# Kernel optimization log

Hardware: AMD Instinct MI355X
Metric: run time of the kernel (lower is better)

## Reference

```python
import jax, jax.numpy as jnp
import numpy as np

B, C, IMG = 32, 3, 224
NP = 14            # patches per side
PS = IMG // NP     # 16
IN_DIM = C * PS * PS  # 768
D = 768
NH = 12
DH = D // NH       # 64
L = 12
MLP = 4 * D        # 3072
OUT = 1000
S = NP * NP + 1    # 197
EPS = 1e-5


def _pos_embedding(seq_len, dim):
    i = jnp.arange(seq_len, dtype=jnp.float32)[:, None]
    j = jnp.arange(dim, dtype=jnp.float32)[None, :]
    je = j - jnp.mod(j, 2.0)  # even: j, odd: j-1
    angle = i / jnp.power(10000.0, je / dim)
    return jnp.where(jnp.mod(j, 2.0) == 0, jnp.sin(angle), jnp.cos(angle))


def setup_inputs() -> dict:
    key = jax.random.key(0)
    ks = jax.random.split(key, 24)
    s = 0.02
    inp = {
        "x": jax.random.normal(ks[0], (B, C, IMG, IMG), jnp.float32),
        "cls_emb": jax.random.normal(ks[1], (1, 1, D), jnp.float32),
        "pos": _pos_embedding(S, D),
        "Wmap": jax.random.normal(ks[2], (IN_DIM, D), jnp.float32) * s,
        "bmap": jnp.zeros((D,), jnp.float32),
        "ln1_g": jnp.ones((L, D), jnp.float32),
        "ln1_b": jnp.zeros((L, D), jnp.float32),
        "Wq": jax.random.normal(ks[3], (L, NH, DH, DH), jnp.float32) * s,
        "bq": jnp.zeros((L, NH, DH), jnp.float32),
        "Wk": jax.random.normal(ks[4], (L, NH, DH, DH), jnp.float32) * s,
        "bk": jnp.zeros((L, NH, DH), jnp.float32),
        "Wv": jax.random.normal(ks[5], (L, NH, DH, DH), jnp.float32) * s,
        "bv": jnp.zeros((L, NH, DH), jnp.float32),
        "ln2_g": jnp.ones((L, D), jnp.float32),
        "ln2_b": jnp.zeros((L, D), jnp.float32),
        "W1": jax.random.normal(ks[6], (L, D, MLP), jnp.float32) * s,
        "b1": jnp.zeros((L, MLP), jnp.float32),
        "W2": jax.random.normal(ks[7], (L, MLP, D), jnp.float32) * s,
        "b2": jnp.zeros((L, D), jnp.float32),
        "Wc": jax.random.normal(ks[8], (D, OUT), jnp.float32) * s,
        "bc": jnp.zeros((OUT,), jnp.float32),
    }
    return inp


def _layernorm(x, g, b):
    mu = jnp.mean(x, axis=-1, keepdims=True)
    var = jnp.var(x, axis=-1, keepdims=True)
    return (x - mu) * jax.lax.rsqrt(var + EPS) * g + b


def _patchify(x):
    # [B,C,H,W] -> [B, NP*NP, C*PS*PS], flatten order (c, h, w) per patch
    n = x.shape[0]
    x = x.reshape(n, C, NP, PS, NP, PS)
    x = jnp.transpose(x, (0, 2, 4, 1, 3, 5))  # [B, ph, pw, C, PS, PS]
    return x.reshape(n, NP * NP, IN_DIM)


def reference(x, cls_emb, pos, Wmap, bmap, ln1_g, ln1_b, Wq, bq, Wk, bk, Wv, bv,
              ln2_g, ln2_b, W1, b1, W2, b2, Wc, bc):
    patches = _patchify(x)
    tokens = patches @ Wmap + bmap  # [B, NP*NP, D]
    tokens = jnp.concatenate([jnp.broadcast_to(cls_emb, (x.shape[0], 1, D)), tokens], axis=1)
    out = tokens + pos  # [B, S, D]
    scale = 1.0 / jnp.sqrt(jnp.float32(DH))
    for l in range(L):
        xn = _layernorm(out, ln1_g[l], ln1_b[l])
        xh = xn.reshape(xn.shape[0], S, NH, DH)
        q = jnp.einsum('bshd,hed->bshe', xh, Wq[l]) + bq[l]
        k = jnp.einsum('bshd,hed->bshe', xh, Wk[l]) + bk[l]
        v = jnp.einsum('bshd,hed->bshe', xh, Wv[l]) + bv[l]
        att = jax.nn.softmax(jnp.einsum('bqhd,bkhd->bhqk', q, k) * scale, axis=-1)
        attn_out = jnp.einsum('bhqk,bkhd->bqhd', att, v).reshape(out.shape)
        out = out + attn_out
        xn2 = _layernorm(out, ln2_g[l], ln2_b[l])
        h = jax.nn.gelu(xn2 @ W1[l] + b1[l], approximate=False)
        out = out + (h @ W2[l] + b2[l])
    cls = out[:, 0]
    return jax.nn.softmax(cls @ Wc + bc, axis=-1)
```

## Files before the change

kernel.cpp:

```cpp
#include <hip/hip_runtime.h>
#include <hip/hip_bf16.h>
#include <math.h>

#define VB   32
#define VD   768
#define VNH  12
#define VDH  64
#define VL   12
#define VMLP 3072
#define VOUT 1000
#define VS   197
#define VNPAT 196

typedef _Float16 half8 __attribute__((ext_vector_type(8)));
typedef _Float16 half4 __attribute__((ext_vector_type(4)));
typedef float f32x4 __attribute__((ext_vector_type(4)));

static __device__ __forceinline__ unsigned short f2h(float f) {
  _Float16 h = (_Float16)f;
  return __builtin_bit_cast(unsigned short, h);
}
static __device__ __forceinline__ float h2f(unsigned short u) {
  return (float)__builtin_bit_cast(_Float16, u);
}

__global__ __launch_bounds__(256) void patchify_kernel(
    const float* __restrict__ x, unsigned short* __restrict__ P) {
  int bp = blockIdx.x;
  int b = bp / VNPAT, p = bp - b * VNPAT;
  int py = p / 14, px = p - py * 14;
  int t = threadIdx.x;
  int iy = t >> 4, ix = t & 15;
#pragma unroll
  for (int c = 0; c < 3; c++) {
    float val = x[(((size_t)(b * 3 + c) * 224) + (py * 16 + iy)) * 224 + px * 16 + ix];
    P[(size_t)bp * 768 + c * 256 + t] = f2h(val);
  }
}

__global__ __launch_bounds__(256) void transpose_kernel(
    const float* __restrict__ W, unsigned short* __restrict__ WT,
    int K, int N) {
  __shared__ float ts[64][65];
  int n0 = blockIdx.x * 64, k0 = blockIdx.y * 64;
  const float* Wl = W + (size_t)blockIdx.z * K * N;
  unsigned short* WTl = WT + (size_t)blockIdx.z * K * N;
  int t = threadIdx.x;
  int r = t >> 4, c4 = (t & 15) * 4;
#pragma unroll
  for (int p = 0; p < 4; ++p) {
    int row = p * 16 + r;
    float4 v = *(const float4*)(Wl + (size_t)(k0 + row) * N + n0 + c4);
    ts[row][c4 + 0] = v.x; ts[row][c4 + 1] = v.y;
    ts[row][c4 + 2] = v.z; ts[row][c4 + 3] = v.w;
  }
  __syncthreads();
#pragma unroll
  for (int p = 0; p < 4; ++p) {
    int n = p * 16 + r;
    ushort4 o;
    o.x = f2h(ts[c4 + 0][n]);
    o.y = f2h(ts[c4 + 1][n]);
    o.z = f2h(ts[c4 + 2][n]);
    o.w = f2h(ts[c4 + 3][n]);
    *(ushort4*)(WTl + (size_t)(n0 + n) * K + k0 + c4) = o;
  }
}

__global__ __launch_bounds__(256) void pack_qkv_kernel(
    const float* __restrict__ Wq, const float* __restrict__ Wk,
    const float* __restrict__ Wv, unsigned short* __restrict__ Wp) {
  size_t idx = (size_t)blockIdx.x * 256 + threadIdx.x;
  int d = idx & 63;
  size_t r = idx >> 6;
  int n = (int)(r % 192);
  size_t lh = r / 192;
  int which = n >> 6, e = n & 63;
  const float* W = which == 0 ? Wq : which == 1 ? Wk : Wv;
  Wp[idx] = f2h(W[(lh * 64 + e) * 64 + d]);
}

__global__ __launch_bounds__(256) void addpos_kernel(
    const float* __restrict__ cls, const float* __restrict__ pos,
    float* __restrict__ out) {
  int bs = blockIdx.x;
  int s = bs % VS;
  int t = threadIdx.x;
  size_t o = (size_t)bs * VD;
#pragma unroll
  for (int j = 0; j < 3; j++) {
    int d = j * 256 + t;
    if (s == 0) out[o + d] = cls[d] + pos[d];
    else        out[o + d] += pos[(size_t)s * VD + d];
  }
}

__global__ __launch_bounds__(256) void ln_kernel(
    const float* __restrict__ x, unsigned short* __restrict__ y,
    const float* __restrict__ g, const float* __restrict__ b) {
  int row = blockIdx.x;
  int t = threadIdx.x;
  const float* xr = x + (size_t)row * VD;
  float v0 = xr[t], v1 = xr[t + 256], v2 = xr[t + 512];
  float s = v0 + v1 + v2;
  float ss = v0 * v0 + v1 * v1 + v2 * v2;
#pragma unroll
  for (int off = 32; off; off >>= 1) {
    s  += __shfl_down(s, off);
    ss += __shfl_down(ss, off);
  }
  __shared__ float red[10];
  int wid = t >> 6, lane = t & 63;
  if (lane == 0) { red[wid] = s; red[4 + wid] = ss; }
  __syncthreads();
  if (t == 0) {
    float S  = red[0] + red[1] + red[2] + red[3];
    float SS = red[4] + red[5] + red[6] + red[7];
    float mu = S * (1.0f / VD);
    float var = SS * (1.0f / VD) - mu * mu;
    red[8] = mu;
    red[9] = rsqrtf(var + 1e-5f);
  }
  __syncthreads();
  float mu = red[8], rs = red[9];
  unsigned short* yr = y + (size_t)row * VD;
  yr[t]       = f2h((v0 - mu) * rs * g[t]       + b[t]);
  yr[t + 256] = f2h((v1 - mu) * rs * g[t + 256] + b[t + 256]);
  yr[t + 512] = f2h((v2 - mu) * rs * g[t + 512] + b[t + 512]);
}

__global__ __launch_bounds__(256) void qkv_gemm(
    const unsigned short* __restrict__ xn,
    const unsigned short* __restrict__ Wp,
    const float* __restrict__ bq, const float* __restrict__ bk,
    const float* __restrict__ bv,
    unsigned short* __restrict__ qh, unsigned short* __restrict__ kh,
    unsigned short* __restrict__ vt) {
  __shared__ unsigned short As[128 * 72];
  __shared__ unsigned short Bs[192 * 72];
  int h = blockIdx.y;
  int bm = blockIdx.x * 128;
  int t = threadIdx.x;
  int srow = t >> 3;
  int scol = (t & 7) * 8;
#pragma unroll
  for (int p = 0; p < 4; ++p) {
    int row = p * 32 + srow;
    int grow = bm + row;
    uint4 val = make_uint4(0u, 0u, 0u, 0u);
    if (grow < VB * VS)
      val = *(const uint4*)(xn + (size_t)grow * VD + h * 64 + scol);
    *(uint4*)(&As[row * 72 + scol]) = val;
  }
#pragma unroll
  for (int p = 0; p < 6; ++p) {
    int row = p * 32 + srow;
    uint4 val = *(const uint4*)(Wp + ((size_t)h * 192 + row) * 64 + scol);
    *(uint4*)(&Bs[row * 72 + scol]) = val;
  }
  __syncthreads();
  int lane = t & 63, wv = t >> 6;
  int wm = (wv & 1) * 64, wn = (wv >> 1) * 96;
  int l15 = lane & 15, l4 = lane >> 4;
  f32x4 acc[4][6] = {};
#pragma unroll
  for (int kk = 0; kk < 64; kk += 32) {
    half8 af[4], bf[6];
#pragma unroll
    for (int i = 0; i < 4; ++i)
      af[i] = *(const half8*)(&As[(wm + i * 16 + l15) * 72 + kk + l4 * 8]);
#pragma unroll
    for (int j = 0; j < 6; ++j)
      bf[j] = *(const half8*)(&Bs[(wn + j * 16 + l15) * 72 + kk + l4 * 8]);
#pragma unroll
    for (int i = 0; i < 4; ++i)
#pragma unroll
      for (int j = 0; j < 6; ++j)
        acc[i][j] = __builtin_amdgcn_mfma_f32_16x16x32_f16(
            af[i], bf[j], acc[i][j], 0, 0, 0);
  }
#pragma unroll
  for (int j = 0; j < 6; ++j) {
    int n = wn + j * 16 + l15;
    int which = n >> 6, e = n & 63;
    const float* bias = which == 0 ? bq : which == 1 ? bk : bv;
    float bval = bias[h * 64 + e];
#pragma unroll
    for (int i = 0; i < 4; ++i) {
#pragma unroll
      for (int r = 0; r < 4; ++r) {
        int tok = bm + wm + i * 16 + l4 * 4 + r;
        if (tok < VB * VS) {
          int b = tok / VS, s = tok - b * VS;
          size_t bh = (size_t)b * VNH + h;
          unsigned short val = f2h(acc[i][j][r] + bval);
          if (which == 0)      qh[(bh * VS + s) * 64 + e] = val;
          else if (which == 1) kh[(bh * VS + s) * 64 + e] = val;
          else                 vt[(bh * 64 + e) * 208 + s] = val;
        }
      }
    }
  }
}

#define PSTR 212
__global__ __launch_bounds__(256) void attn_mfma(
    const unsigned short* __restrict__ qh,
    const unsigned short* __restrict__ kh,
    const unsigned short* __restrict__ vt,
    float* __restrict__ out) {
  int bh = blockIdx.x;
  int qt = blockIdx.y;
  int t = threadIdx.x;
  int w = t >> 6, lane = t & 63;
  int l15 = lane & 15, l4 = lane >> 4;
  __shared__ unsigned short Pl[4][16 * PSTR];

  int qrow = qt * 64 + w * 16 + l15;
  const unsigned short* qbase = qh + ((size_t)bh * VS) * 64;
  const unsigned short* kbase = kh + ((size_t)bh * VS) * 64;
  half8 qf0 = *(const half8*)(qbase + (size_t)qrow * 64 + l4 * 8);
  half8 qf1 = *(const half8*)(qbase + (size_t)qrow * 64 + 32 + l4 * 8);

  f32x4 S[13];
#pragma unroll
  for (int j = 0; j < 13; ++j) {
    half8 b0 = *(const half8*)(kbase + (size_t)(j * 16 + l15) * 64 + l4 * 8);
    half8 b1 = *(const half8*)(kbase + (size_t)(j * 16 + l15) * 64 + 32 + l4 * 8);
    f32x4 c = {};
    c = __builtin_amdgcn_mfma_f32_16x16x32_f16(qf0, b0, c, 0, 0, 0);
    c = __builtin_amdgcn_mfma_f32_16x16x32_f16(qf1, b1, c, 0, 0, 0);
    S[j] = c;
  }
  float m4[4] = {-3.0e38f, -3.0e38f, -3.0e38f, -3.0e38f};
#pragma unroll
  for (int j = 0; j < 13; ++j) {
#pragma unroll
    for (int r = 0; r < 4; ++r) {
      float s = S[j][r] * 0.125f;
      if (j == 12 && l15 > 4) s = -3.0e38f;
      S[j][r] = s;
      m4[r] = fmaxf(m4[r], s);
    }
  }
#pragma unroll
  for (int off = 1; off < 16; off <<= 1) {
#pragma unroll
    for (int r = 0; r < 4; ++r) m4[r] = fmaxf(m4[r], __shfl_xor(m4[r], off));
  }
  float ls[4] = {0.f, 0.f, 0.f, 0.f};
#pragma unroll
  for (int j = 0; j < 13; ++j) {
#pragma unroll
    for (int r = 0; r < 4; ++r) {
      float p = __expf(S[j][r] - m4[r]);
      S[j][r] = p;
      ls[r] += p;
    }
  }
#pragma unroll
  for (int off = 1; off < 16; off <<= 1) {
#pragma unroll
    for (int r = 0; r < 4; ++r) ls[r] += __shfl_xor(ls[r], off);
  }
  unsigned short* Pw = &Pl[w][0];
#pragma unroll
  for (int j = 0; j < 13; ++j) {
#pragma unroll
    for (int r = 0; r < 4; ++r)
      Pw[(l4 * 4 + r) * PSTR + j * 16 + l15] = f2h(S[j][r]);
  }
  const unsigned short* vbase = vt + (size_t)bh * 64 * 208;
  f32x4 O[4] = {};
#pragma unroll
  for (int jk = 0; jk < 13; ++jk) {
    half4 a = *(const half4*)(Pw + l15 * PSTR + jk * 16 + l4 * 4);
#pragma unroll
    for (int jn = 0; jn < 4; ++jn) {
      half4 b = *(const half4*)(vbase + (size_t)(jn * 16 + l15) * 208 + jk * 16 + l4 * 4);
      O[jn] = __builtin_amdgcn_mfma_f32_16x16x16f16(a, b, O[jn], 0, 0, 0);
    }
  }
  int b = bh / VNH, h = bh - (bh / VNH) * VNH;
  float linv[4];
#pragma unroll
  for (int r = 0; r < 4; ++r) linv[r] = 1.0f / ls[r];
#pragma unroll
  for (int r = 0; r < 4; ++r) {
    int qr = qt * 64 + w * 16 + l4 * 4 + r;
    if (qr < VS) {
      float* op = out + ((size_t)b * VS + qr) * VD + h * VDH;
#pragma unroll
      for (int jn = 0; jn < 4; ++jn)
        op[jn * 16 + l15] += O[jn][r] * linv[r];
    }
  }
}

#define BM 128
#define BN 128
#define BKK 64
#define LDA 72

template <int EPI, int REMAP>
__global__ __launch_bounds__(256) void gemm_h(
    const unsigned short* __restrict__ A,
    const unsigned short* __restrict__ Bt,
    const float* __restrict__ bias, float* __restrict__ C,
    int M, int N, int K) {
  __shared__ unsigned short As[BM * LDA];
  __shared__ unsigned short Bs[BN * LDA];
  int t = threadIdx.x;
  int bm = blockIdx.y * BM, bn = blockIdx.x * BN;
  int lane = t & 63, wv = t >> 6;
  int wm = (wv & 1) * 64, wn = (wv >> 1) * 64;
  int l15 = lane & 15, l4 = lane >> 4;
  f32x4 acc[4][4] = {};
  int srow = t >> 3;
  int scol = (t & 7) * 8;
  for (int k0 = 0; k0 < K; k0 += BKK) {
#pragma unroll
    for (int p = 0; p < 4; ++p) {
      int row = p * 32 + srow;
      int grow = bm + row;
      uint4 val = make_uint4(0u, 0u, 0u, 0u);
      if (grow < M) val = *(const uint4*)(A + (size_t)grow * K + k0 + scol);
      *(uint4*)(&As[row * LDA + scol]) = val;
    }
#pragma unroll
    for (int p = 0; p < 4; ++p) {
      int row = p * 32 + srow;
      uint4 val = *(const uint4*)(Bt + (size_t)(bn + row) * K + k0 + scol);
      *(uint4*)(&Bs[row * LDA + scol]) = val;
    }
    __syncthreads();
#pragma unroll
    for (int kk = 0; kk < BKK; kk += 32) {
      half8 af[4], bf[4];
#pragma unroll
      for (int i = 0; i < 4; ++i)
        af[i] = *(const half8*)(&As[(wm + i * 16 + l15) * LDA + kk + l4 * 8]);
#pragma unroll
      for (int j = 0; j < 4; ++j)
        bf[j] = *(const half8*)(&Bs[(wn + j * 16 + l15) * LDA + kk + l4 * 8]);
#pragma unroll
      for (int i = 0; i < 4; ++i)
#pragma unroll
        for (int j = 0; j < 4; ++j)
          acc[i][j] = __builtin_amdgcn_mfma_f32_16x16x32_f16(
              af[i], bf[j], acc[i][j], 0, 0, 0);
    }
    __syncthreads();
  }
#pragma unroll
  for (int i = 0; i < 4; ++i) {
#pragma unroll
    for (int j = 0; j < 4; ++j) {
#pragma unroll
      for (int r = 0; r < 4; ++r) {
        int row = bm + wm + i * 16 + l4 * 4 + r;
        int col = bn + wn + j * 16 + l15;
        if (row < M) {
          float val = acc[i][j][r] + bias[col];
          if (EPI == 0) {
            int crow = REMAP ? (row + row / 196 + 1) : row;
            C[(size_t)crow * N + col] = val;
          } else if (EPI == 1) {
            val = 0.5f * val * (1.0f + erff(val * 0.70710678118654752440f));
            ((unsigned short*)C)[(size_t)row * N + col] = f2h(val);
          } else {
            C[(size_t)row * N + col] += val;
          }
        }
      }
    }
  }
}

__global__ __launch_bounds__(256) void cls_kernel(
    const float* __restrict__ out_act, const float* __restrict__ Wc,
    const float* __restrict__ bc, float* __restrict__ y) {
  int b = blockIdx.x;
  int t = threadIdx.x;
  __shared__ float xs[768];
  __shared__ float logit[VOUT];
  __shared__ float red[10];
  const float* xr = out_act + (size_t)b * VS * VD;
  xs[t] = xr[t]; xs[t + 256] = xr[t + 256]; xs[t + 512] = xr[t + 512];
  __syncthreads();
  for (int j0 = 0; j0 < VOUT; j0 += 256) {
    int j = j0 + t;
    if (j < VOUT) {
      float acc = bc[j];
      for (int d = 0; d < VD; d++) acc += xs[d] * Wc[(size_t)d * VOUT + j];
      logit[j] = acc;
    }
  }
  __syncthreads();
  float m = -1e30f;
  for (int j = t; j < VOUT; j += 256) m = fmaxf(m, logit[j]);
#pragma unroll
  for (int off = 32; off; off >>= 1) m = fmaxf(m, __shfl_down(m, off));
  if ((t & 63) == 0) red[t >> 6] = m;
  __syncthreads();
  if (t == 0) red[8] = fmaxf(fmaxf(red[0], red[1]), fmaxf(red[2], red[3]));
  __syncthreads();
  float M = red[8];
  float s = 0.f;
  for (int j = t; j < VOUT; j += 256) {
    float e = expf(logit[j] - M);
    logit[j] = e;
    s += e;
  }
#pragma unroll
  for (int off = 32; off; off >>= 1) s += __shfl_down(s, off);
  if ((t & 63) == 0) red[4 + (t >> 6)] = s;
  __syncthreads();
  if (t == 0) red[9] = red[4] + red[5] + red[6] + red[7];
  __syncthreads();
  float inv = 1.0f / red[9];
  for (int j = t; j < VOUT; j += 256) y[(size_t)b * VOUT + j] = logit[j] * inv;
}

extern "C" void kernel_launch(void* const* d_in, const int* in_sizes, int n_in,
                              void* d_out, int out_size, void* d_ws, size_t ws_size,
                              hipStream_t stream) {
  const float* x      = (const float*)d_in[0];
  const float* cls    = (const float*)d_in[1];
  const float* pos    = (const float*)d_in[2];
  const float* Wmap   = (const float*)d_in[3];
  const float* bmap   = (const float*)d_in[4];
  const float* ln1_g  = (const float*)d_in[5];
  const float* ln1_b  = (const float*)d_in[6];
  const float* Wq     = (const float*)d_in[7];
  const float* bq     = (const float*)d_in[8];
  const float* Wk     = (const float*)d_in[9];
  const float* bk     = (const float*)d_in[10];
  const float* Wv     = (const float*)d_in[11];
  const float* bv     = (const float*)d_in[12];
  const float* ln2_g  = (const float*)d_in[13];
  const float* ln2_b  = (const float*)d_in[14];
  const float* W1     = (const float*)d_in[15];
  const float* b1     = (const float*)d_in[16];
  const float* W2     = (const float*)d_in[17];
  const float* b2     = (const float*)d_in[18];
  const float* Wc     = (const float*)d_in[19];
  const float* bc     = (const float*)d_in[20];
  float* yout = (float*)d_out;

  const size_t nBS  = (size_t)VB * VS;
  const size_t nBSD = nBS * VD;
  const size_t nQK  = (size_t)VB * VNH * VS * 64;
  char* base = (char*)d_ws;
  size_t off = 0;
  float* out_act = (float*)(base + off);      off += nBSD * 4;
  unsigned short* xnb = (unsigned short*)(base + off); off += nBSD * 2;
  unsigned short* qhb = (unsigned short*)(base + off); off += nQK * 2 + 65536;
  unsigned short* khb = (unsigned short*)(base + off); off += nQK * 2 + 65536;
  unsigned short* vtb = (unsigned short*)(base + off); off += (size_t)VB * VNH * 64 * 208 * 2;
  unsigned short* hbuf = (unsigned short*)(base + off); off += nBS * VMLP * 2;
  unsigned short* wmapT = (unsigned short*)(base + off); off += (size_t)VD * VD * 2;
  unsigned short* w1T = (unsigned short*)(base + off);   off += (size_t)VL * VMLP * VD * 2;
  unsigned short* w2T = (unsigned short*)(base + off);   off += (size_t)VL * VD * VMLP * 2;
  unsigned short* wqkv = (unsigned short*)(base + off);  off += (size_t)VL * VNH * 192 * 64 * 2;

  transpose_kernel<<<dim3(12, 12, 1), 256, 0, stream>>>(Wmap, wmapT, VD, VD);
  transpose_kernel<<<dim3(48, 12, VL), 256, 0, stream>>>(W1, w1T, VD, VMLP);
  transpose_kernel<<<dim3(12, 48, VL), 256, 0, stream>>>(W2, w2T, VMLP, VD);
  pack_qkv_kernel<<<(VL * VNH * 192 * 64) / 256, 256, 0, stream>>>(Wq, Wk, Wv, wqkv);

  patchify_kernel<<<VB * VNPAT, 256, 0, stream>>>(x, hbuf);
  gemm_h<0, 1><<<dim3(VD / BN, (VB * VNPAT) / BM), 256, 0, stream>>>(
      hbuf, wmapT, bmap, out_act, VB * VNPAT, VD, VD);
  addpos_kernel<<<(int)nBS, 256, 0, stream>>>(cls, pos, out_act);

  for (int l = 0; l < VL; l++) {
    ln_kernel<<<(int)nBS, 256, 0, stream>>>(out_act, xnb,
                                            ln1_g + (size_t)l * VD,
                                            ln1_b + (size_t)l * VD);
    qkv_gemm<<<dim3(50, VNH), 256, 0, stream>>>(
        xnb, wqkv + (size_t)l * VNH * 192 * 64,
        bq + (size_t)l * VNH * VDH, bk + (size_t)l * VNH * VDH,
        bv + (size_t)l * VNH * VDH, qhb, khb, vtb);
    attn_mfma<<<dim3(VB * VNH, 4), 256, 0, stream>>>(qhb, khb, vtb, out_act);
    ln_kernel<<<(int)nBS, 256, 0, stream>>>(out_act, xnb,
                                            ln2_g + (size_t)l * VD,
                                            ln2_b + (size_t)l * VD);
    gemm_h<1, 0><<<dim3(VMLP / BN, ((int)nBS + BM - 1) / BM), 256, 0, stream>>>(
        xnb, w1T + (size_t)l * VMLP * VD, b1 + (size_t)l * VMLP,
        (float*)hbuf, (int)nBS, VMLP, VD);
    gemm_h<2, 0><<<dim3(VD / BN, ((int)nBS + BM - 1) / BM), 256, 0, stream>>>(
        hbuf, w2T + (size_t)l * VD * VMLP, b2 + (size_t)l * VD,
        out_act, (int)nBS, VD, VMLP);
  }
  cls_kernel<<<VB, 256, 0, stream>>>(out_act, Wc, bc, yout);
}
```

Baseline: 4.290 ms.

## Use direct global-to-LDS loads in GEMM, split-K MLP2, split classifier

The GEMM tile loads now use global_load_lds with 16-byte transfers, so data goes straight into LDS without passing through registers. The LDS rows also lose their padding, which risks bank conflicts on the fragment reads. The second MLP GEMM is split over K into two partial buffers, and a separate reduce kernel adds them, the bias and the residual; this adds blocks but costs extra memory traffic. A kernel now zeroes the padded tail of the transposed V buffer each layer. The classifier is split into a parallel logits kernel and a softmax kernel.

```diff
diff --git a/kernel.cpp b/kernel.cpp
--- a/kernel.cpp
+++ b/kernel.cpp
@@ -22,6 +22,12 @@
 }
 static __device__ __forceinline__ float h2f(unsigned short u) {
   return (float)__builtin_bit_cast(_Float16, u);
+}
+
+static __device__ __forceinline__ void gload_lds16(const void* g, void* l) {
+  __builtin_amdgcn_global_load_lds(
+      (const __attribute__((address_space(1))) unsigned int*)g,
+      (__attribute__((address_space(3))) unsigned int*)l, 16, 0, 0);
 }
 
 __global__ __launch_bounds__(256) void patchify_kernel(
@@ -203,6 +209,13 @@
   }
 }
 
+__global__ __launch_bounds__(256) void vt_ztail(unsigned short* __restrict__ vt) {
+  int i = blockIdx.x * 256 + threadIdx.x;
+  int c = i % 11;
+  int rd = i / 11;
+  vt[(size_t)rd * 208 + 197 + c] = 0;
+}
+
 #define PSTR 212
 __global__ __launch_bounds__(256) void attn_mfma(
     const unsigned short* __restrict__ qh,
@@ -297,52 +310,42 @@
   }
 }
 
-#define BM 128
-#define BN 128
-#define BKK 64
-#define LDA 72
-
 template <int EPI, int REMAP>
 __global__ __launch_bounds__(256) void gemm_h(
     const unsigned short* __restrict__ A,
     const unsigned short* __restrict__ Bt,
     const float* __restrict__ bias, float* __restrict__ C,
-    int M, int N, int K) {
-  __shared__ unsigned short As[BM * LDA];
-  __shared__ unsigned short Bs[BN * LDA];
-  int t = threadIdx.x;
-  int bm = blockIdx.y * BM, bn = blockIdx.x * BN;
-  int lane = t & 63, wv = t >> 6;
-  int wm = (wv & 1) * 64, wn = (wv >> 1) * 64;
+    int M, int N, int K, int KS) {
+  __shared__ unsigned short As[128 * 64];
+  __shared__ unsigned short Bs[128 * 64];
+  int t = threadIdx.x;
+  int bm = blockIdx.y * 128, bn = blockIdx.x * 128;
+  int lane = t & 63, w = t >> 6;
+  int wm = (w & 1) * 64, wn = (w >> 1) * 64;
   int l15 = lane & 15, l4 = lane >> 4;
+  int lrow = lane >> 3, lcol = (lane & 7) * 8;
   f32x4 acc[4][4] = {};
-  int srow = t >> 3;
-  int scol = (t & 7) * 8;
-  for (int k0 = 0; k0 < K; k0 += BKK) {
+  int kbeg = blockIdx.z * KS;
+  if (EPI == 3) C += (size_t)blockIdx.z * M * N;
+  for (int k0 = kbeg; k0 < kbeg + KS; k0 += 64) {
 #pragma unroll
     for (int p = 0; p < 4; ++p) {
-      int row = p * 32 + srow;
-      int grow = bm + row;
-      uint4 val = make_uint4(0u, 0u, 0u, 0u);
-      if (grow < M) val = *(const uint4*)(A + (size_t)grow * K + k0 + scol);
-      *(uint4*)(&As[row * LDA + scol]) = val;
-    }
-#pragma unroll
-    for (int p = 0; p < 4; ++p) {
-      int row = p * 32 + srow;
-      uint4 val = *(const uint4*)(Bt + (size_t)(bn + row) * K + k0 + scol);
-      *(uint4*)(&Bs[row * LDA + scol]) = val;
+      int r0 = w * 32 + p * 8;
+      int ga = bm + r0;
+      if (ga > M - 8) ga = M - 8;
+      gload_lds16(A + (size_t)(ga + lrow) * K + k0 + lcol, &As[r0 * 64]);
+      gload_lds16(Bt + (size_t)(bn + r0 + lrow) * K + k0 + lcol, &Bs[r0 * 64]);
     }
     __syncthreads();
 #pragma unroll
-    for (int kk = 0; kk < BKK; kk += 32) {
+    for (int kk = 0; kk < 64; kk += 32) {
       half8 af[4], bf[4];
 #pragma unroll
       for (int i = 0; i < 4; ++i)
-        af[i] = *(const half8*)(&As[(wm + i * 16 + l15) * LDA + kk + l4 * 8]);
+        af[i] = *(const half8*)(&As[(wm + i * 16 + l15) * 64 + kk + l4 * 8]);
 #pragma unroll
       for (int j = 0; j < 4; ++j)
-        bf[j] = *(const half8*)(&Bs[(wn + j * 16 + l15) * LDA + kk + l4 * 8]);
+        bf[j] = *(const half8*)(&Bs[(wn + j * 16 + l15) * 64 + kk + l4 * 8]);
 #pragma unroll
       for (int i = 0; i < 4; ++i)
 #pragma unroll
@@ -361,15 +364,19 @@
         int row = bm + wm + i * 16 + l4 * 4 + r;
         int col = bn + wn + j * 16 + l15;
         if (row < M) {
-          float val = acc[i][j][r] + bias[col];
-          if (EPI == 0) {
-            int crow = REMAP ? (row + row / 196 + 1) : row;
-            C[(size_t)crow * N + col] = val;
-          } else if (EPI == 1) {
-            val = 0.5f * val * (1.0f + erff(val * 0.70710678118654752440f));
-            ((unsigned short*)C)[(size_t)row * N + col] = f2h(val);
+          if (EPI == 3) {
+            C[(size_t)row * N + col] = acc[i][j][r];
           } else {
-            C[(size_t)row * N + col] += val;
+            float val = acc[i][j][r] + bias[col];
+            if (EPI == 0) {
+              int crow = REMAP ? (row + row / 196 + 1) : row;
+              C[(size_t)crow * N + col] = val;
+            } else if (EPI == 1) {
+              val = 0.5f * val * (1.0f + erff(val * 0.70710678118654752440f));
+              ((unsigned short*)C)[(size_t)row * N + col] = f2h(val);
+            } else {
+              C[(size_t)row * N + col] += val;
+            }
           }
         }
       }
@@ -377,25 +384,48 @@
   }
 }
 
-__global__ __launch_bounds__(256) void cls_kernel(
+__global__ __launch_bounds__(256) void mlp2_reduce(
+    const float* __restrict__ p0, const float* __restrict__ p1,
+    const float* __restrict__ bias, float* __restrict__ out) {
+  size_t idx = ((size_t)blockIdx.x * 256 + threadIdx.x) * 4;
+  int col = (int)(idx % VD);
+  float4 a = *(const float4*)(p0 + idx);
+  float4 b = *(const float4*)(p1 + idx);
+  float4 bi = *(const float4*)(bias + col);
+  float4 o = *(const float4*)(out + idx);
+  o.x += a.x + b.x + bi.x;
+  o.y += a.y + b.y + bi.y;
+  o.z += a.z + b.z + bi.z;
+  o.w += a.w + b.w + bi.w;
+  *(float4*)(out + idx) = o;
+}
+
+__global__ __launch_bounds__(256) void cls_logits(
     const float* __restrict__ out_act, const float* __restrict__ Wc,
-    const float* __restrict__ bc, float* __restrict__ y) {
+    const float* __restrict__ bc, float* __restrict__ lbuf) {
+  int b = blockIdx.y;
+  int n0 = blockIdx.x * 250;
+  int t = threadIdx.x;
+  __shared__ float xs[768];
+  const float* xr = out_act + (size_t)b * VS * VD;
+  xs[t] = xr[t]; xs[t + 256] = xr[t + 256]; xs[t + 512] = xr[t + 512];
+  __syncthreads();
+  if (t < 250) {
+    int col = n0 + t;
+    float acc = bc[col];
+#pragma unroll 4
+    for (int d = 0; d < VD; ++d) acc += xs[d] * Wc[(size_t)d * VOUT + col];
+    lbuf[(size_t)b * VOUT + col] = acc;
+  }
+}
+
+__global__ __launch_bounds__(256) void cls_softmax(
+    const float* __restrict__ lbuf, float* __restrict__ y) {
   int b = blockIdx.x;
   int t = threadIdx.x;
-  __shared__ float xs[768];
   __shared__ float logit[VOUT];
   __shared__ float red[10];
-  const float* xr = out_act + (size_t)b * VS * VD;
-  xs[t] = xr[t]; xs[t + 256] = xr[t + 256]; xs[t + 512] = xr[t + 512];
-  __syncthreads();
-  for (int j0 = 0; j0 < VOUT; j0 += 256) {
-    int j = j0 + t;
-    if (j < VOUT) {
-      float acc = bc[j];
-      for (int d = 0; d < VD; d++) acc += xs[d] * Wc[(size_t)d * VOUT + j];
-      logit[j] = acc;
-    }
-  }
+  for (int j = t; j < VOUT; j += 256) logit[j] = lbuf[(size_t)b * VOUT + j];
   __syncthreads();
   float m = -1e30f;
   for (int j = t; j < VOUT; j += 256) m = fmaxf(m, logit[j]);
@@ -463,6 +493,8 @@
   unsigned short* w1T = (unsigned short*)(base + off);   off += (size_t)VL * VMLP * VD * 2;
   unsigned short* w2T = (unsigned short*)(base + off);   off += (size_t)VL * VD * VMLP * 2;
   unsigned short* wqkv = (unsigned short*)(base + off);  off += (size_t)VL * VNH * 192 * 64 * 2;
+  float* part = (float*)xnb;
+  float* lbuf = (float*)qhb;
 
   transpose_kernel<<<dim3(12, 12, 1), 256, 0, stream>>>(Wmap, wmapT, VD, VD);
   transpose_kernel<<<dim3(48, 12, VL), 256, 0, stream>>>(W1, w1T, VD, VMLP);
@@ -470,8 +502,8 @@
   pack_qkv_kernel<<<(VL * VNH * 192 * 64) / 256, 256, 0, stream>>>(Wq, Wk, Wv, wqkv);
 
   patchify_kernel<<<VB * VNPAT, 256, 0, stream>>>(x, hbuf);
-  gemm_h<0, 1><<<dim3(VD / BN, (VB * VNPAT) / BM), 256, 0, stream>>>(
-      hbuf, wmapT, bmap, out_act, VB * VNPAT, VD, VD);
+  gemm_h<0, 1><<<dim3(6, 49), 256, 0, stream>>>(
+      hbuf, wmapT, bmap, out_act, VB * VNPAT, VD, VD, VD);
   addpos_kernel<<<(int)nBS, 256, 0, stream>>>(cls, pos, out_act);
 
   for (int l = 0; l < VL; l++) {
@@ -482,16 +514,20 @@
         xnb, wqkv + (size_t)l * VNH * 192 * 64,
         bq + (size_t)l * VNH * VDH, bk + (size_t)l * VNH * VDH,
         bv + (size_t)l * VNH * VDH, qhb, khb, vtb);
+    vt_ztail<<<(VB * VNH * 64 * 11) / 256, 256, 0, stream>>>(vtb);
     attn_mfma<<<dim3(VB * VNH, 4), 256, 0, stream>>>(qhb, khb, vtb, out_act);
     ln_kernel<<<(int)nBS, 256, 0, stream>>>(out_act, xnb,
                                             ln2_g + (size_t)l * VD,
                                             ln2_b + (size_t)l * VD);
-    gemm_h<1, 0><<<dim3(VMLP / BN, ((int)nBS + BM - 1) / BM), 256, 0, stream>>>(
+    gemm_h<1, 0><<<dim3(24, 50), 256, 0, stream>>>(
         xnb, w1T + (size_t)l * VMLP * VD, b1 + (size_t)l * VMLP,
-        (float*)hbuf, (int)nBS, VMLP, VD);
-    gemm_h<2, 0><<<dim3(VD / BN, ((int)nBS + BM - 1) / BM), 256, 0, stream>>>(
-        hbuf, w2T + (size_t)l * VD * VMLP, b2 + (size_t)l * VD,
-        out_act, (int)nBS, VD, VMLP);
-  }
-  cls_kernel<<<VB, 256, 0, stream>>>(out_act, Wc, bc, yout);
-}
+        (float*)hbuf, (int)nBS, VMLP, VD, VD);
+    gemm_h<3, 0><<<dim3(6, 50, 2), 256, 0, stream>>>(
+        hbuf, w2T + (size_t)l * VD * VMLP, nullptr,
+        part, (int)nBS, VD, VMLP, VMLP / 2);
+    mlp2_reduce<<<(int)(nBSD / 1024), 256, 0, stream>>>(
+        part, part + nBSD, b2 + (size_t)l * VD, out_act);
+  }
+  cls_logits<<<dim3(4, VB), 256, 0, stream>>>(out_act, Wc, bc, lbuf);
+  cls_softmax<<<VB, 256, 0, stream>>>(lbuf, yout);
+}
```

Measured after the change: 4.071 ms. 5.1% less time.
